# Kernel tuning notes

Hardware: AMD Instinct MI355X
Metric: run time of the kernel (lower is better)

The kernel has to match this reference:

```python
import jax, jax.numpy as jnp
import numpy as np
from jax import lax

SEQ_LEN = 12
E = 64        # embedding_dim
HD = 128      # h_dim
G = 32        # number of scenes (seq_start_end rows)
P = 32        # pedestrians per scene
B = G * P     # total batch
BOT = 1024    # bottleneck_dim
MLP = 1024    # mlp_dim
BN_S = 1.0 / np.sqrt(1.0 + 1e-5)  # eval BatchNorm1d with running mean 0 / var 1


def setup_inputs():
    key = jax.random.key(0)
    ks = jax.random.split(key, 32)
    r = lambda k, s, sc=0.1: (jax.random.normal(k, s, jnp.float32) * sc)
    starts = np.arange(G, dtype=np.int32) * P
    sse = jnp.asarray(np.stack([starts, starts + P], 1))
    return {
        'last_pos': r(ks[0], (B, 2), 1.0),
        'last_pos_rel': r(ks[1], (B, 2), 1.0),
        'h0': r(ks[2], (1, B, HD), 1.0),
        'c0': r(ks[3], (1, B, HD), 1.0),
        'vx': r(ks[4], (8, B), 1.0),
        'vy': r(ks[5], (8, B), 1.0),
        'agent_type': jax.random.uniform(ks[6], (8, B, 1), jnp.float32),
        'seq_start_end': sse,
        # decoder params
        'W_sp': r(ks[7], (2, E)), 'b_sp': r(ks[8], (E,)),
        'W_ih': r(ks[9], (E, 4 * HD)), 'W_hh': r(ks[10], (HD, 4 * HD)),
        'b_ih': r(ks[11], (4 * HD,)), 'b_hh': r(ks[12], (4 * HD,)),
        'W_h2p': r(ks[13], (HD, 2)), 'b_h2p': r(ks[14], (2,)),
        # AttenPoolNet params
        'Wp_sp': r(ks[15], (2, E)), 'bp_sp': r(ks[16], (E,)),
        'Wp_vel': r(ks[17], (2, E)), 'bp_vel': r(ks[18], (E,)),
        'Wp_at': r(ks[19], (6, E)), 'bp_at': r(ks[20], (E,)),
        'Wa1': r(ks[21], (E, MLP)), 'ba1': r(ks[22], (MLP,)),
        'Wa2': r(ks[23], (MLP, 1)), 'ba2': r(ks[24], (1,)),
        'Wm1': r(ks[25], (E + HD, 512)), 'bm1': r(ks[26], (512,)),
        'Wm2': r(ks[27], (512, BOT)), 'bm2': r(ks[28], (BOT,)),
        # decoder post-pool mlp: [h+bottleneck, mlp_dim, h]
        'Wd1': r(ks[29], (HD + BOT, MLP)), 'bd1': r(ks[30], (MLP,)),
        'Wd2': r(ks[31], (MLP, HD)), 'bd2': jnp.zeros((HD,), jnp.float32),
    }


def _bnrelu(x):
    # make_mlp: Linear -> BatchNorm1d (eval, mean 0 / var 1) -> ReLU
    return jax.nn.relu(x * BN_S)


def reference(last_pos, last_pos_rel, h0, c0, vx, vy, agent_type, seq_start_end,
              W_sp, b_sp, W_ih, W_hh, b_ih, b_hh, W_h2p, b_h2p,
              Wp_sp, bp_sp, Wp_vel, bp_vel, Wp_at, bp_at,
              Wa1, ba1, Wa2, ba2, Wm1, bm1, Wm2, bm2,
              Wd1, bd1, Wd2, bd2):
    g = seq_start_end.shape[0]
    p = last_pos.shape[0] // g

    at0 = agent_type[0].reshape(g, p, 1)               # agent_type[0,:,:] per group
    at_rep = jnp.repeat(at0, 6, axis=-1)               # .repeat(num_ped, 6) width expansion
    at_emb = at_rep @ Wp_at + bp_at                    # (g,p,E), index j (tiled over i)
    vel = jnp.stack([vx[-1], vy[-1]], -1).reshape(g, p, 2)
    _vel_emb = vel @ Wp_vel + bp_vel                   # computed in source, unused downstream

    def pool(h2d, pos):
        Hh = h2d.reshape(g, p, HD)
        pg = pos.reshape(g, p, 2)
        # rel[s,i,j] = pos[s,j] - pos[s,i]
        rel = pg[:, None, :, :] - pg[:, :, None, :]
        rel_emb = rel @ Wp_sp + bp_sp                  # (g,p,p,E)
        a = _bnrelu(rel_emb @ Wa1 + ba1)               # (g,p,p,MLP)
        s = _bnrelu(a @ Wa2 + ba2)                     # (g,p,p,1)
        w = jax.nn.softmax(s, axis=-1)                 # torch softmax(dim=1) over size-1 axis -> ones
        base = jnp.concatenate([Hh, at_emb], -1)       # (g,p,192), index j
        wt = base[:, None, :, :] * (0.05 * w)          # (g,p,p,192)
        m = _bnrelu(wt @ Wm1 + bm1)
        m = _bnrelu(m @ Wm2 + bm2)                     # (g,p,p,BOT)
        return m.max(axis=2).reshape(g * p, BOT)       # max over j per tile index i

    def lstm(x, h, c):
        gates = x @ W_ih + h @ W_hh + b_ih + b_hh
        i, f, gg, o = jnp.split(gates, 4, axis=-1)
        c = jax.nn.sigmoid(f) * c + jax.nn.sigmoid(i) * jnp.tanh(gg)
        h = jax.nn.sigmoid(o) * jnp.tanh(c)
        return h, c

    def step(carry, _):
        lp, di, h, c = carry
        h, c = lstm(di, h, c)
        rel = h @ W_h2p + b_h2p
        cur = rel + lp
        ph = pool(h, cur)
        dh = _bnrelu(jnp.concatenate([h, ph], -1) @ Wd1 + bd1)
        dh = _bnrelu(dh @ Wd2 + bd2)
        di = rel @ W_sp + b_sp
        return (cur, di, dh, c), rel

    init = (last_pos, last_pos_rel @ W_sp + b_sp, h0[0], c0[0])
    (lp, di, h, c), rels = lax.scan(step, init, None, length=SEQ_LEN)
    return rels, h[None]  # (seq_len,B,2), (1,B,HD)
```

## Files before the change

kernel.cpp:

```cpp
#include <hip/hip_runtime.h>
#include <math.h>

#define BN_SF 0.9999950000374997f

typedef __attribute__((ext_vector_type(8))) short short8v;
typedef __attribute__((ext_vector_type(4))) float float4v;

__device__ __forceinline__ float sigm(float x) { return 1.0f / (1.0f + expf(-x)); }

__device__ __forceinline__ short f2bf(float x) {
    unsigned u = __builtin_bit_cast(unsigned, x);
    unsigned r = (u + 0x7fffu + ((u >> 16) & 1u)) >> 16;
    return (short)r;
}
__device__ __forceinline__ float bf2f(short h) {
    unsigned u = ((unsigned)(unsigned short)h) << 16;
    return __builtin_bit_cast(float, u);
}

struct SetupP {
    const float *Wm2, *Wd1, *Wd2, *Wm1, *Wih, *Whh, *Wpat, *bpat, *bm1, *c0;
    const float *Wsp, *bsp, *bih, *bhh;
    short *Wm2s, *Wd1f, *Wd2f, *Wm1f, *WghHi, *WghLo;
    float *uv, *cbuf, *fc;
};

__global__ __launch_bounds__(256) void k_setup(SetupP p) {
    __shared__ float tile[32][65];
    __shared__ float rw2[64], su[4][64], sv[4][64];
    int b = blockIdx.x, t = threadIdx.x;

    if (b < 960) {
        const float* src; short* dst; short* dst2 = nullptr;
        int K, N, tm; float scale = 1.f;
        if (b < 256)      { src = p.Wm2; dst = p.Wm2s; K = 512;  N = 1024; tm = b; }
        else if (b < 832) { src = p.Wd1; dst = p.Wd1f; K = 1152; N = 1024; tm = b - 256; }
        else if (b < 896) { src = p.Wd2; dst = p.Wd2f; K = 1024; N = 128;  tm = b - 832; }
        else if (b < 928) { src = p.Wm1; dst = p.Wm1f; K = 128;  N = 512;  tm = b - 896; scale = 0.05f; }
        else              { src = p.Whh; dst = p.WghHi; dst2 = p.WghLo; K = 128; N = 512; tm = b - 928; }
        int tiles_n = N >> 6;
        int kt = tm / tiles_n, nt = tm - kt * tiles_n;
        for (int i = t; i < 2048; i += 256) {
            int r = i >> 6, c = i & 63;
            tile[r][c] = scale * src[(size_t)(kt * 32 + r) * N + nt * 64 + c];
        }
        __syncthreads();
        int lane = t & 63, ntgl = t >> 6;
        int ntg = nt * 4 + ntgl;
        size_t off = (size_t)ntg * ((K >> 5) * 512) + (size_t)kt * 512 + lane * 8;
        int kl = (lane >> 4) << 3, nl = ntgl * 16 + (lane & 15);
        short8v vh, vl;
#pragma unroll
        for (int j = 0; j < 8; ++j) {
            float v = tile[kl + j][nl];
            short hi = f2bf(v);
            vh[j] = hi; vl[j] = f2bf(v - bf2f(hi));
        }
        *(short8v*)(dst + off) = vh;
        if (dst2) *(short8v*)(dst2 + off) = vl;
    } else {
        int i0 = (b - 960) * 256 + t;
        ((float4*)p.cbuf)[i0] = ((const float4*)p.c0)[i0];
        ((float4*)p.cbuf)[i0 + 16384] = ((const float4*)p.c0)[i0 + 16384];
    }

    if (b < 8) {
        int lane = t & 63, seg = t >> 6;
        if (t < 64) { float s = 0.f; for (int k = 0; k < 6; ++k) s += p.Wpat[k * 64 + t]; rw2[t] = s; }
        __syncthreads();
        int c = b * 64 + lane;
        float u = 0.f, v = 0.f;
        for (int e = seg * 16; e < seg * 16 + 16; ++e) {
            float wg = p.Wm1[(size_t)(128 + e) * 512 + c];
            u += rw2[e] * wg; v += p.bpat[e] * wg;
        }
        su[seg][lane] = u; sv[seg][lane] = v;
        __syncthreads();
        if (seg == 0) {
            u = su[0][lane] + su[1][lane] + su[2][lane] + su[3][lane];
            v = sv[0][lane] + sv[1][lane] + sv[2][lane] + sv[3][lane];
            p.uv[c] = 0.05f * u; p.uv[512 + c] = 0.05f * v + p.bm1[c];
        }
    }
    if (b == 8) {
        for (int c = t; c < 512; c += 256) {
            float f0 = 0.f, f1 = 0.f, cc = 0.f;
            for (int e = 0; e < 64; ++e) {
                float wv = p.Wih[(size_t)e * 512 + c];
                f0 += p.Wsp[e] * wv; f1 += p.Wsp[64 + e] * wv; cc += p.bsp[e] * wv;
            }
            p.fc[c] = f0; p.fc[512 + c] = f1; p.fc[1024 + c] = cc + p.bih[c] + p.bhh[c];
        }
    }
}

__global__ __launch_bounds__(512, 4) void k_step(
    const short* __restrict__ WghHi, const short* __restrict__ WghLo,
    const short* __restrict__ Wm1f, const short* __restrict__ Wd2f,
    const short* __restrict__ Wd1f,
    const float* __restrict__ Whp, const float* __restrict__ bhp,
    const float* __restrict__ bd1, const float* __restrict__ bd2,
    const float* __restrict__ at0, const float* __restrict__ uv,
    const float* __restrict__ fc,
    const float* __restrict__ h0, const float* __restrict__ relsrc,
    const float* __restrict__ phwp, const short* __restrict__ hf_in, int first,
    float* __restrict__ cbuf, short* __restrict__ hf_out,
    short* __restrict__ m1s, float* __restrict__ outrel) {
    __shared__ float sgu[16 * 512];
    __shared__ float sh[16][128];
    __shared__ float phws[1024];
    __shared__ short xfh[4 * 512];
    __shared__ short xfl[4 * 512];
    __shared__ short xm[4 * 512];
    __shared__ float srelp[16][2];
    __shared__ float sat[16];
    short* dh1L = (short*)sgu;
    float* sg = sgu;

    int t = threadIdx.x, b = blockIdx.x;
    int l = t & 63, w = t >> 6;
    int s = b >> 1, mt = b & 1, r0 = b * 16;
    int rbase = (l >> 4) << 2;

    if (t < 16) sat[t] = at0[r0 + t];
    if (t < 32) { int row = t >> 1, d = t & 1; srelp[row][d] = relsrc[(r0 + row) * 2 + d]; }

    if (first) {
        for (int i = t; i < 16 * 128; i += 512) sh[i >> 7][i & 127] = h0[r0 * 128 + i];
        __syncthreads();
    } else {
        for (int i = t; i < 1024; i += 512) {
            float v = bd1[i];
#pragma unroll
            for (int ct = 0; ct < 8; ++ct) v += phwp[(size_t)s * 8192 + ct * 1024 + i];
            phws[i] = v;
        }
        __syncthreads();
        short8v Ah[4];
#pragma unroll
        for (int kc = 0; kc < 4; ++kc)
            Ah[kc] = *(const short8v*)(hf_in + (size_t)b * 2048 + kc * 512 + l * 8);
#pragma unroll 1
        for (int q2 = 0; q2 < 4; ++q2) {
            short8v B[2][4];
#pragma unroll
            for (int qq = 0; qq < 2; ++qq)
#pragma unroll
                for (int kc = 0; kc < 4; ++kc)
                    B[qq][kc] = *(const short8v*)(Wd1f + (size_t)(w * 8 + q2 * 2 + qq) * 18432 + kc * 512 + l * 8);
            float4v acc2[2];
#pragma unroll
            for (int qq = 0; qq < 2; ++qq) {
                int col = (w * 8 + q2 * 2 + qq) * 16 + (l & 15);
                float pv = phws[col];
                acc2[qq] = (float4v){pv, pv, pv, pv};
            }
#pragma unroll
            for (int kc = 0; kc < 4; ++kc)
#pragma unroll
                for (int qq = 0; qq < 2; ++qq)
                    acc2[qq] = __builtin_amdgcn_mfma_f32_16x16x32_bf16(Ah[kc], B[qq][kc], acc2[qq], 0, 0, 0);
#pragma unroll
            for (int qq = 0; qq < 2; ++qq) {
                int col = (w * 8 + q2 * 2 + qq) * 16 + (l & 15);
                int kcD = col >> 5, jD = col & 7, lD = ((col & 31) >> 3) << 4;
#pragma unroll
                for (int r = 0; r < 4; ++r) {
                    float v = fmaxf(BN_SF * acc2[qq][r], 0.f);
                    dh1L[kcD * 512 + (rbase + r + lD) * 8 + jD] = f2bf(v);
                }
            }
        }
        __syncthreads();
        float4v hacc = {0.f, 0.f, 0.f, 0.f};
        const short* ap = dh1L + l * 8;
        const short* bp = Wd2f + (size_t)w * 16384 + l * 8;
#pragma unroll 1
        for (int kt = 0; kt < 4; ++kt) {
            short8v B[8], A[8];
#pragma unroll
            for (int kk = 0; kk < 8; ++kk) B[kk] = *(const short8v*)(bp + (kt * 8 + kk) * 512);
#pragma unroll
            for (int kk = 0; kk < 8; ++kk) A[kk] = *(const short8v*)(ap + (kt * 8 + kk) * 512);
#pragma unroll
            for (int kk = 0; kk < 8; ++kk)
                hacc = __builtin_amdgcn_mfma_f32_16x16x32_bf16(A[kk], B[kk], hacc, 0, 0, 0);
        }
        int col = w * 16 + (l & 15);
        float bb2 = bd2[col];
        __syncthreads();
#pragma unroll
        for (int r = 0; r < 4; ++r)
            sh[rbase + r][col] = fmaxf(BN_SF * (hacc[r] + bb2), 0.f);
        __syncthreads();
    }

    for (int i = t; i < 4 * 512; i += 512) {
        int pos = i & 511, kc = i >> 9;
        int ll = pos >> 3, j = pos & 7;
        int row = ll & 15, kh = kc * 32 + ((ll >> 4) << 3) + j;
        float v = sh[row][kh];
        short hi = f2bf(v);
        xfh[i] = hi;
        xfl[i] = f2bf(v - bf2f(hi));
    }
    __syncthreads();

    {
        float4v ga[4];
#pragma unroll
        for (int q = 0; q < 4; ++q) {
            int col = (w * 4 + q) * 16 + (l & 15);
            float f0 = fc[col], f1 = fc[512 + col], cc = fc[1024 + col];
#pragma unroll
            for (int r = 0; r < 4; ++r)
                ga[q][r] = srelp[rbase + r][0] * f0 + srelp[rbase + r][1] * f1 + cc;
        }
#pragma unroll 1
        for (int kt = 0; kt < 2; ++kt) {
            short8v BH[2][4], BL[2][4], AH[2], AL[2];
#pragma unroll
            for (int kk = 0; kk < 2; ++kk) {
                int kcx = kt * 2 + kk;
#pragma unroll
                for (int q = 0; q < 4; ++q) {
                    int nf = w * 4 + q;
                    BH[kk][q] = *(const short8v*)(WghHi + (size_t)nf * 2048 + kcx * 512 + l * 8);
                    BL[kk][q] = *(const short8v*)(WghLo + (size_t)nf * 2048 + kcx * 512 + l * 8);
                }
                AH[kk] = *(const short8v*)(&xfh[kcx * 512 + l * 8]);
                AL[kk] = *(const short8v*)(&xfl[kcx * 512 + l * 8]);
            }
#pragma unroll
            for (int kk = 0; kk < 2; ++kk)
#pragma unroll
                for (int q = 0; q < 4; ++q) {
                    ga[q] = __builtin_amdgcn_mfma_f32_16x16x32_bf16(AH[kk], BH[kk][q], ga[q], 0, 0, 0);
                    ga[q] = __builtin_amdgcn_mfma_f32_16x16x32_bf16(AH[kk], BL[kk][q], ga[q], 0, 0, 0);
                    ga[q] = __builtin_amdgcn_mfma_f32_16x16x32_bf16(AL[kk], BH[kk][q], ga[q], 0, 0, 0);
                }
        }
#pragma unroll
        for (int q = 0; q < 4; ++q) {
            int col = (w * 4 + q) * 16 + (l & 15);
#pragma unroll
            for (int r = 0; r < 4; ++r)
                sg[(rbase + r) * 512 + col] = ga[q][r];
        }
    }
    __syncthreads();

    for (int i = t; i < 16 * 128; i += 512) {
        int row = i >> 7, j = i & 127;
        float gi = sg[row * 512 + j], gf = sg[row * 512 + j + 128];
        float gg = sg[row * 512 + j + 256], go = sg[row * 512 + j + 384];
        float cn = sigm(gf) * cbuf[(r0 + row) * 128 + j] + sigm(gi) * tanhf(gg);
        float hn = sigm(go) * tanhf(cn);
        cbuf[(r0 + row) * 128 + j] = cn;
        sh[row][j] = hn;
    }
    __syncthreads();

    if (t < 256) {
        int row = t >> 4, d = (t >> 3) & 1, seg = t & 7;
        float v = 0.f;
#pragma unroll
        for (int kk = 0; kk < 16; ++kk) {
            int k = seg * 16 + kk;
            v += sh[row][k] * Whp[k * 2 + d];
        }
        v += __shfl_xor(v, 1, 64); v += __shfl_xor(v, 2, 64); v += __shfl_xor(v, 4, 64);
        if (seg == 0) outrel[(r0 + row) * 2 + d] = v + bhp[d];
    }
    for (int i = t; i < 4 * 512; i += 512) {
        int pos = i & 511, kc = i >> 9;
        int ll = pos >> 3, j = pos & 7;
        int row = ll & 15, k = kc * 32 + ((ll >> 4) << 3) + j;
        short hv = f2bf(sh[row][k]);
        xm[i] = hv;
        hf_out[(size_t)b * 2048 + i] = hv;
    }
    __syncthreads();

    {
        float4v ma[4] = {{0,0,0,0},{0,0,0,0},{0,0,0,0},{0,0,0,0}};
        short8v A[4], B[4][4];
#pragma unroll
        for (int kc = 0; kc < 4; ++kc) {
#pragma unroll
            for (int q = 0; q < 4; ++q)
                B[kc][q] = *(const short8v*)(Wm1f + (size_t)(w * 4 + q) * 2048 + kc * 512 + l * 8);
            A[kc] = *(const short8v*)(&xm[kc * 512 + l * 8]);
        }
#pragma unroll
        for (int kc = 0; kc < 4; ++kc)
#pragma unroll
            for (int q = 0; q < 4; ++q)
                ma[q] = __builtin_amdgcn_mfma_f32_16x16x32_bf16(A[kc], B[kc][q], ma[q], 0, 0, 0);
#pragma unroll
        for (int q = 0; q < 4; ++q) {
            int col = (w * 4 + q) * 16 + (l & 15);
            float uc = uv[col], vc = uv[512 + col];
#pragma unroll
            for (int r = 0; r < 4; ++r) {
                int rowC = rbase + r;
                float m1v = fmaxf(BN_SF * (ma[q][r] + sat[rowC] * uc + vc), 0.f);
                int kcD = col >> 5;
                int laneD = rowC + (((col & 31) >> 3) << 4);
                m1s[(size_t)s * 16384 + kcD * 1024 + mt * 512 + laneD * 8 + (col & 7)] = f2bf(m1v);
            }
        }
    }
}

__global__ __launch_bounds__(512, 4) void k_m2(const short* __restrict__ m1s,
                                               const short* __restrict__ Wm2s,
                                               const short* __restrict__ Wd1f,
                                               const float* __restrict__ bm2,
                                               float* __restrict__ phwp) {
    __shared__ short sphb[128];
    int t = threadIdx.x, l = t & 63, w = t >> 6;
    int s = blockIdx.x >> 3, ct = blockIdx.x & 7;

    {
        int nf = ct * 8 + w;
        const short* ap = m1s + (size_t)s * 16384 + l * 8;
        const short* bp = Wm2s + (size_t)nf * 8192 + l * 8;
        float4v acc0 = {0,0,0,0}, acc1 = {0,0,0,0};
#pragma unroll 1
        for (int kt = 0; kt < 4; ++kt) {
            short8v A0[4], A1[4], B[4];
#pragma unroll
            for (int kk = 0; kk < 4; ++kk) {
                int kc = kt * 4 + kk;
                B[kk] = *(const short8v*)(bp + kc * 512);
                A0[kk] = *(const short8v*)(ap + kc * 1024);
                A1[kk] = *(const short8v*)(ap + kc * 1024 + 512);
            }
#pragma unroll
            for (int kk = 0; kk < 4; ++kk) {
                acc0 = __builtin_amdgcn_mfma_f32_16x16x32_bf16(A0[kk], B[kk], acc0, 0, 0, 0);
                acc1 = __builtin_amdgcn_mfma_f32_16x16x32_bf16(A1[kk], B[kk], acc1, 0, 0, 0);
            }
        }
        float m = acc0[0];
#pragma unroll
        for (int ri = 1; ri < 4; ++ri) m = fmaxf(m, acc0[ri]);
#pragma unroll
        for (int ri = 0; ri < 4; ++ri) m = fmaxf(m, acc1[ri]);
        m = fmaxf(m, __shfl_xor(m, 16, 64));
        m = fmaxf(m, __shfl_xor(m, 32, 64));
        if (l < 16) {
            int col = nf * 16 + l;
            sphb[w * 16 + l] = f2bf(fmaxf(BN_SF * (m + bm2[col]), 0.f));
        }
    }
    __syncthreads();

    {
        short8v Ap[4];
#pragma unroll
        for (int kk = 0; kk < 4; ++kk)
            Ap[kk] = *(const short8v*)(sphb + kk * 32 + ((l >> 4) << 3));
#pragma unroll 1
        for (int q2 = 0; q2 < 4; ++q2) {
            short8v B[2][4];
#pragma unroll
            for (int qq = 0; qq < 2; ++qq)
#pragma unroll
                for (int kk = 0; kk < 4; ++kk)
                    B[qq][kk] = *(const short8v*)(Wd1f + (size_t)(w * 8 + q2 * 2 + qq) * 18432
                                                  + (size_t)(4 + ct * 4 + kk) * 512 + l * 8);
            float4v acc2[2] = {{0,0,0,0},{0,0,0,0}};
#pragma unroll
            for (int kk = 0; kk < 4; ++kk)
#pragma unroll
                for (int qq = 0; qq < 2; ++qq)
                    acc2[qq] = __builtin_amdgcn_mfma_f32_16x16x32_bf16(Ap[kk], B[qq][kk], acc2[qq], 0, 0, 0);
            if (l < 16) {
#pragma unroll
                for (int qq = 0; qq < 2; ++qq) {
                    int nf_p = w * 8 + q2 * 2 + qq;
                    phwp[(size_t)s * 8192 + ct * 1024 + nf_p * 16 + l] = acc2[qq][0];
                }
            }
        }
    }
}

__global__ __launch_bounds__(512, 4) void k_hfin(const short* __restrict__ Wd2f,
                                                 const short* __restrict__ Wd1f,
                                                 const float* __restrict__ bd1,
                                                 const float* __restrict__ bd2,
                                                 const float* __restrict__ phwp,
                                                 const short* __restrict__ hf,
                                                 float* __restrict__ outh) {
    __shared__ float phws[1024];
    __shared__ short dh1L[16384];
    int t = threadIdx.x, b = blockIdx.x;
    int l = t & 63, w = t >> 6;
    int s = b >> 1, rbase = (l >> 4) << 2;

    for (int i = t; i < 1024; i += 512) {
        float v = bd1[i];
#pragma unroll
        for (int ct = 0; ct < 8; ++ct) v += phwp[(size_t)s * 8192 + ct * 1024 + i];
        phws[i] = v;
    }
    __syncthreads();
    short8v Ah[4];
#pragma unroll
    for (int kc = 0; kc < 4; ++kc)
        Ah[kc] = *(const short8v*)(hf + (size_t)b * 2048 + kc * 512 + l * 8);
#pragma unroll 1
    for (int q2 = 0; q2 < 4; ++q2) {
        short8v B[2][4];
#pragma unroll
        for (int qq = 0; qq < 2; ++qq)
#pragma unroll
            for (int kc = 0; kc < 4; ++kc)
                B[qq][kc] = *(const short8v*)(Wd1f + (size_t)(w * 8 + q2 * 2 + qq) * 18432 + kc * 512 + l * 8);
        float4v acc2[2];
#pragma unroll
        for (int qq = 0; qq < 2; ++qq) {
            int col = (w * 8 + q2 * 2 + qq) * 16 + (l & 15);
            float pv = phws[col];
            acc2[qq] = (float4v){pv, pv, pv, pv};
        }
#pragma unroll
        for (int kc = 0; kc < 4; ++kc)
#pragma unroll
            for (int qq = 0; qq < 2; ++qq)
                acc2[qq] = __builtin_amdgcn_mfma_f32_16x16x32_bf16(Ah[kc], B[qq][kc], acc2[qq], 0, 0, 0);
#pragma unroll
        for (int qq = 0; qq < 2; ++qq) {
            int col = (w * 8 + q2 * 2 + qq) * 16 + (l & 15);
            int kcD = col >> 5, jD = col & 7, lD = ((col & 31) >> 3) << 4;
#pragma unroll
            for (int r = 0; r < 4; ++r) {
                float v = fmaxf(BN_SF * acc2[qq][r], 0.f);
                dh1L[kcD * 512 + (rbase + r + lD) * 8 + jD] = f2bf(v);
            }
        }
    }
    __syncthreads();
    float4v hacc = {0.f, 0.f, 0.f, 0.f};
    const short* ap = dh1L + l * 8;
    const short* bp = Wd2f + (size_t)w * 16384 + l * 8;
#pragma unroll 1
    for (int kt = 0; kt < 4; ++kt) {
        short8v B[8], A[8];
#pragma unroll
        for (int kk = 0; kk < 8; ++kk) B[kk] = *(const short8v*)(bp + (kt * 8 + kk) * 512);
#pragma unroll
        for (int kk = 0; kk < 8; ++kk) A[kk] = *(const short8v*)(ap + (kt * 8 + kk) * 512);
#pragma unroll
        for (int kk = 0; kk < 8; ++kk)
            hacc = __builtin_amdgcn_mfma_f32_16x16x32_bf16(A[kk], B[kk], hacc, 0, 0, 0);
    }
    int col = w * 16 + (l & 15);
    float bb2 = bd2[col];
#pragma unroll
    for (int r = 0; r < 4; ++r)
        outh[(b * 16 + rbase + r) * 128 + col] = fmaxf(BN_SF * (hacc[r] + bb2), 0.f);
}

extern "C" void kernel_launch(void* const* d_in, const int* in_sizes, int n_in,
                              void* d_out, int out_size, void* d_ws, size_t ws_size,
                              hipStream_t stream) {
    const float* lpr   = (const float*)d_in[1];
    const float* h0    = (const float*)d_in[2];
    const float* c0    = (const float*)d_in[3];
    const float* at0   = (const float*)d_in[6];
    const float* W_sp  = (const float*)d_in[8];
    const float* b_sp  = (const float*)d_in[9];
    const float* W_ih  = (const float*)d_in[10];
    const float* W_hh  = (const float*)d_in[11];
    const float* b_ih  = (const float*)d_in[12];
    const float* b_hh  = (const float*)d_in[13];
    const float* W_h2p = (const float*)d_in[14];
    const float* b_h2p = (const float*)d_in[15];
    const float* Wp_at = (const float*)d_in[20];
    const float* bp_at = (const float*)d_in[21];
    const float* Wm1   = (const float*)d_in[26];
    const float* bm1   = (const float*)d_in[27];
    const float* Wm2   = (const float*)d_in[28];
    const float* bm2   = (const float*)d_in[29];
    const float* Wd1   = (const float*)d_in[30];
    const float* bd1   = (const float*)d_in[31];
    const float* Wd2   = (const float*)d_in[32];
    const float* bd2   = (const float*)d_in[33];
    float* out = (float*)d_out;

    float* ws    = (float*)d_ws;
    float* uv    = ws;
    float* fc    = uv + 1024;
    float* cbuf  = fc + 1536;
    float* phwp  = cbuf + 131072;
    short* hf    = (short*)(phwp + 262144);
    short* m1s   = hf + 131072;
    short* Wm2s  = m1s + 524288;
    short* Wd1f  = Wm2s + 524288;
    short* Wd2f  = Wd1f + 1179648;
    short* Wm1f  = Wd2f + 131072;
    short* WghHi = Wm1f + 65536;
    short* WghLo = WghHi + 65536;

    SetupP sp;
    sp.Wm2 = Wm2; sp.Wd1 = Wd1; sp.Wd2 = Wd2; sp.Wm1 = Wm1;
    sp.Wih = W_ih; sp.Whh = W_hh; sp.Wpat = Wp_at; sp.bpat = bp_at; sp.bm1 = bm1;
    sp.c0 = c0; sp.Wsp = W_sp; sp.bsp = b_sp; sp.bih = b_ih; sp.bhh = b_hh;
    sp.Wm2s = Wm2s; sp.Wd1f = Wd1f; sp.Wd2f = Wd2f;
    sp.Wm1f = Wm1f; sp.WghHi = WghHi; sp.WghLo = WghLo;
    sp.uv = uv; sp.cbuf = cbuf; sp.fc = fc;

    k_setup<<<1024, 256, 0, stream>>>(sp);

    for (int t = 0; t < 12; ++t) {
        const float* relsrc = (t == 0) ? lpr : (out + (size_t)(t - 1) * 2048);
        k_step<<<64, 512, 0, stream>>>(WghHi, WghLo, Wm1f, Wd2f, Wd1f,
                                       W_h2p, b_h2p, bd1, bd2, at0, uv, fc,
                                       h0, relsrc, phwp, hf, (t == 0) ? 1 : 0,
                                       cbuf, hf, m1s, out + (size_t)t * 2048);
        k_m2<<<256, 512, 0, stream>>>(m1s, Wm2s, Wd1f, bm2, phwp);
    }
    k_hfin<<<64, 512, 0, stream>>>(Wd2f, Wd1f, bd1, bd2, phwp, hf, out + 24576);
}
```

Before: 328.3 us.

## Fuse per-step kernels into one persistent kernel with flag-based inter-block sync

```diff
diff --git a/kernel.cpp b/kernel.cpp
--- a/kernel.cpp
+++ b/kernel.cpp
@@ -16,6 +16,33 @@
 __device__ __forceinline__ float bf2f(short h) {
     unsigned u = ((unsigned)(unsigned short)h) << 16;
     return __builtin_bit_cast(float, u);
+}
+
+__device__ __forceinline__ void st_ag64(void* p, unsigned long long v) {
+    __hip_atomic_store((unsigned long long*)p, v, __ATOMIC_RELAXED, __HIP_MEMORY_SCOPE_AGENT);
+}
+__device__ __forceinline__ unsigned long long ld_ag64(const void* p) {
+    return __hip_atomic_load((const unsigned long long*)p, __ATOMIC_RELAXED, __HIP_MEMORY_SCOPE_AGENT);
+}
+__device__ __forceinline__ void st_ag32f(float* p, float v) {
+    __hip_atomic_store((unsigned*)p, __builtin_bit_cast(unsigned, v), __ATOMIC_RELAXED, __HIP_MEMORY_SCOPE_AGENT);
+}
+__device__ __forceinline__ short8v ld_ag_frag(const short* p) {
+    unsigned long long a = ld_ag64(p), c = ld_ag64(p + 4);
+    short8v v;
+    ((unsigned long long*)&v)[0] = a;
+    ((unsigned long long*)&v)[1] = c;
+    return v;
+}
+__device__ __forceinline__ void waitge(int* f, int target) {
+    long it = 0;
+    while (__hip_atomic_load(f, __ATOMIC_RELAXED, __HIP_MEMORY_SCOPE_AGENT) < target) {
+        __builtin_amdgcn_s_sleep(1);
+        if (++it > (1L << 26)) break;
+    }
+}
+__device__ __forceinline__ void bump_release(int* f) {
+    __hip_atomic_fetch_add(f, 1, __ATOMIC_RELEASE, __HIP_MEMORY_SCOPE_AGENT);
 }
 
 struct SetupP {
@@ -23,6 +50,7 @@
     const float *Wsp, *bsp, *bih, *bhh;
     short *Wm2s, *Wd1f, *Wd2f, *Wm1f, *WghHi, *WghLo;
     float *uv, *cbuf, *fc;
+    int *flags;
 };
 
 __global__ __launch_bounds__(256) void k_setup(SetupP p) {
@@ -92,54 +120,342 @@
             p.fc[c] = f0; p.fc[512 + c] = f1; p.fc[1024 + c] = cc + p.bih[c] + p.bhh[c];
         }
     }
-}
-
-__global__ __launch_bounds__(512, 4) void k_step(
-    const short* __restrict__ WghHi, const short* __restrict__ WghLo,
-    const short* __restrict__ Wm1f, const short* __restrict__ Wd2f,
-    const short* __restrict__ Wd1f,
-    const float* __restrict__ Whp, const float* __restrict__ bhp,
-    const float* __restrict__ bd1, const float* __restrict__ bd2,
-    const float* __restrict__ at0, const float* __restrict__ uv,
-    const float* __restrict__ fc,
-    const float* __restrict__ h0, const float* __restrict__ relsrc,
-    const float* __restrict__ phwp, const short* __restrict__ hf_in, int first,
-    float* __restrict__ cbuf, short* __restrict__ hf_out,
-    short* __restrict__ m1s, float* __restrict__ outrel) {
+    if (b == 9) {
+        if (t < 64) p.flags[t] = 0;
+    }
+}
+
+struct PersistP {
+    const short *WghHi, *WghLo, *Wm1f, *Wd2f, *Wd1f, *Wm2s;
+    const float *Whp, *bhp, *bd1, *bd2, *at0, *uv, *fc, *h0, *lpr, *bm2;
+    float *cbuf;
+    short *hf;
+    short *m1s;
+    float *phwp;
+    int *m1rdy, *phwrdy;
+    float *out;
+};
+
+__global__ __launch_bounds__(512) void k_persist(PersistP p) {
     __shared__ float sgu[16 * 512];
     __shared__ float sh[16][128];
     __shared__ float phws[1024];
-    __shared__ short xfh[4 * 512];
-    __shared__ short xfl[4 * 512];
-    __shared__ short xm[4 * 512];
+    __shared__ short xfh[2048];
+    __shared__ short xfl[2048];
+    __shared__ short xm[2048];
     __shared__ float srelp[16][2];
     __shared__ float sat[16];
+    __shared__ short sphb[128];
     short* dh1L = (short*)sgu;
     float* sg = sgu;
+    short* m1stage = (short*)sgu;
 
     int t = threadIdx.x, b = blockIdx.x;
     int l = t & 63, w = t >> 6;
+    int rbase = (l >> 4) << 2;
+    int s2 = b >> 3, ct = b & 7;
+    bool isStep = (b < 64);
     int s = b >> 1, mt = b & 1, r0 = b * 16;
-    int rbase = (l >> 4) << 2;
-
-    if (t < 16) sat[t] = at0[r0 + t];
-    if (t < 32) { int row = t >> 1, d = t & 1; srelp[row][d] = relsrc[(r0 + row) * 2 + d]; }
-
-    if (first) {
-        for (int i = t; i < 16 * 128; i += 512) sh[i >> 7][i & 127] = h0[r0 * 128 + i];
-        __syncthreads();
-    } else {
-        for (int i = t; i < 1024; i += 512) {
-            float v = bd1[i];
-#pragma unroll
-            for (int ct = 0; ct < 8; ++ct) v += phwp[(size_t)s * 8192 + ct * 1024 + i];
-            phws[i] = v;
+
+    if (isStep && t < 16) sat[t] = p.at0[r0 + t];
+
+    for (int st = 0; st < 12; ++st) {
+        if (isStep) {
+            if (st == 0) {
+                for (int i = t; i < 2048; i += 512) sh[i >> 7][i & 127] = p.h0[r0 * 128 + i];
+                if (t < 32) { int row = t >> 1, d = t & 1; srelp[row][d] = p.lpr[(r0 + row) * 2 + d]; }
+                __syncthreads();
+            } else {
+                if (t == 0) waitge(p.phwrdy + s, 8 * st);
+                __syncthreads();
+                {
+                    float a0 = p.bd1[t * 2], a1 = p.bd1[t * 2 + 1];
+#pragma unroll
+                    for (int cc = 0; cc < 8; ++cc) {
+                        unsigned long long v = ld_ag64(&p.phwp[(size_t)s * 8192 + cc * 1024 + t * 2]);
+                        float2 f = __builtin_bit_cast(float2, v);
+                        a0 += f.x; a1 += f.y;
+                    }
+                    phws[t * 2] = a0; phws[t * 2 + 1] = a1;
+                }
+                if (t < 32) {
+                    int row = t >> 1, d = t & 1;
+                    srelp[row][d] = p.out[(size_t)(st - 1) * 2048 + (r0 + row) * 2 + d];
+                }
+                __syncthreads();
+                short8v Ah[4];
+#pragma unroll
+                for (int kc = 0; kc < 4; ++kc)
+                    Ah[kc] = *(const short8v*)(p.hf + (size_t)b * 2048 + kc * 512 + l * 8);
+#pragma unroll 1
+                for (int q2 = 0; q2 < 4; ++q2) {
+                    short8v B[2][4];
+#pragma unroll
+                    for (int qq = 0; qq < 2; ++qq)
+#pragma unroll
+                        for (int kc = 0; kc < 4; ++kc)
+                            B[qq][kc] = *(const short8v*)(p.Wd1f + (size_t)(w * 8 + q2 * 2 + qq) * 18432 + kc * 512 + l * 8);
+                    float4v acc2[2];
+#pragma unroll
+                    for (int qq = 0; qq < 2; ++qq) {
+                        int col = (w * 8 + q2 * 2 + qq) * 16 + (l & 15);
+                        float pv = phws[col];
+                        acc2[qq] = (float4v){pv, pv, pv, pv};
+                    }
+#pragma unroll
+                    for (int kc = 0; kc < 4; ++kc)
+#pragma unroll
+                        for (int qq = 0; qq < 2; ++qq)
+                            acc2[qq] = __builtin_amdgcn_mfma_f32_16x16x32_bf16(Ah[kc], B[qq][kc], acc2[qq], 0, 0, 0);
+#pragma unroll
+                    for (int qq = 0; qq < 2; ++qq) {
+                        int col = (w * 8 + q2 * 2 + qq) * 16 + (l & 15);
+                        int kcD = col >> 5, jD = col & 7, lD = ((col & 31) >> 3) << 4;
+#pragma unroll
+                        for (int r = 0; r < 4; ++r) {
+                            float v = fmaxf(BN_SF * acc2[qq][r], 0.f);
+                            dh1L[kcD * 512 + (rbase + r + lD) * 8 + jD] = f2bf(v);
+                        }
+                    }
+                }
+                __syncthreads();
+                float4v hacc = {0.f, 0.f, 0.f, 0.f};
+                const short* ap = dh1L + l * 8;
+                const short* bp = p.Wd2f + (size_t)w * 16384 + l * 8;
+#pragma unroll 1
+                for (int kt = 0; kt < 4; ++kt) {
+                    short8v B[8], A[8];
+#pragma unroll
+                    for (int kk = 0; kk < 8; ++kk) B[kk] = *(const short8v*)(bp + (kt * 8 + kk) * 512);
+#pragma unroll
+                    for (int kk = 0; kk < 8; ++kk) A[kk] = *(const short8v*)(ap + (kt * 8 + kk) * 512);
+#pragma unroll
+                    for (int kk = 0; kk < 8; ++kk)
+                        hacc = __builtin_amdgcn_mfma_f32_16x16x32_bf16(A[kk], B[kk], hacc, 0, 0, 0);
+                }
+                int col = w * 16 + (l & 15);
+                float bb2 = p.bd2[col];
+                __syncthreads();
+#pragma unroll
+                for (int r = 0; r < 4; ++r)
+                    sh[rbase + r][col] = fmaxf(BN_SF * (hacc[r] + bb2), 0.f);
+                __syncthreads();
+            }
+
+            for (int i = t; i < 2048; i += 512) {
+                int pos = i & 511, kc = i >> 9;
+                int ll = pos >> 3, j = pos & 7;
+                int row = ll & 15, kh = kc * 32 + ((ll >> 4) << 3) + j;
+                float v = sh[row][kh];
+                short hi = f2bf(v);
+                xfh[i] = hi;
+                xfl[i] = f2bf(v - bf2f(hi));
+            }
+            __syncthreads();
+
+            {
+                float4v ga[4];
+#pragma unroll
+                for (int qg = 0; qg < 4; ++qg) {
+                    int col = (w * 4 + qg) * 16 + (l & 15);
+                    float f0 = p.fc[col], f1 = p.fc[512 + col], cc = p.fc[1024 + col];
+#pragma unroll
+                    for (int r = 0; r < 4; ++r)
+                        ga[qg][r] = srelp[rbase + r][0] * f0 + srelp[rbase + r][1] * f1 + cc;
+                }
+#pragma unroll 1
+                for (int kt = 0; kt < 2; ++kt) {
+                    short8v BH[2][4], BL[2][4], AH[2], AL[2];
+#pragma unroll
+                    for (int kk = 0; kk < 2; ++kk) {
+                        int kcx = kt * 2 + kk;
+#pragma unroll
+                        for (int qg = 0; qg < 4; ++qg) {
+                            int nf = w * 4 + qg;
+                            BH[kk][qg] = *(const short8v*)(p.WghHi + (size_t)nf * 2048 + kcx * 512 + l * 8);
+                            BL[kk][qg] = *(const short8v*)(p.WghLo + (size_t)nf * 2048 + kcx * 512 + l * 8);
+                        }
+                        AH[kk] = *(const short8v*)(&xfh[kcx * 512 + l * 8]);
+                        AL[kk] = *(const short8v*)(&xfl[kcx * 512 + l * 8]);
+                    }
+#pragma unroll
+                    for (int kk = 0; kk < 2; ++kk)
+#pragma unroll
+                        for (int qg = 0; qg < 4; ++qg) {
+                            ga[qg] = __builtin_amdgcn_mfma_f32_16x16x32_bf16(AH[kk], BH[kk][qg], ga[qg], 0, 0, 0);
+                            ga[qg] = __builtin_amdgcn_mfma_f32_16x16x32_bf16(AH[kk], BL[kk][qg], ga[qg], 0, 0, 0);
+                            ga[qg] = __builtin_amdgcn_mfma_f32_16x16x32_bf16(AL[kk], BH[kk][qg], ga[qg], 0, 0, 0);
+                        }
+                }
+#pragma unroll
+                for (int qg = 0; qg < 4; ++qg) {
+                    int col = (w * 4 + qg) * 16 + (l & 15);
+#pragma unroll
+                    for (int r = 0; r < 4; ++r)
+                        sg[(rbase + r) * 512 + col] = ga[qg][r];
+                }
+            }
+            __syncthreads();
+
+            for (int i = t; i < 2048; i += 512) {
+                int row = i >> 7, j = i & 127;
+                float gi = sg[row * 512 + j], gf = sg[row * 512 + j + 128];
+                float gg = sg[row * 512 + j + 256], go = sg[row * 512 + j + 384];
+                float cn = sigm(gf) * p.cbuf[(r0 + row) * 128 + j] + sigm(gi) * tanhf(gg);
+                float hn = sigm(go) * tanhf(cn);
+                p.cbuf[(r0 + row) * 128 + j] = cn;
+                sh[row][j] = hn;
+            }
+            __syncthreads();
+
+            if (t < 256) {
+                int row = t >> 4, d = (t >> 3) & 1, seg = t & 7;
+                float v = 0.f;
+#pragma unroll
+                for (int kk = 0; kk < 16; ++kk) {
+                    int k = seg * 16 + kk;
+                    v += sh[row][k] * p.Whp[k * 2 + d];
+                }
+                v += __shfl_xor(v, 1, 64); v += __shfl_xor(v, 2, 64); v += __shfl_xor(v, 4, 64);
+                if (seg == 0) p.out[(size_t)st * 2048 + (r0 + row) * 2 + d] = v + p.bhp[d];
+            }
+            for (int i = t; i < 2048; i += 512) {
+                int pos = i & 511, kc = i >> 9;
+                int ll = pos >> 3, j = pos & 7;
+                int row = ll & 15, k = kc * 32 + ((ll >> 4) << 3) + j;
+                short hv = f2bf(sh[row][k]);
+                xm[i] = hv;
+                p.hf[(size_t)b * 2048 + i] = hv;
+            }
+            __syncthreads();
+
+            {
+                float4v ma[4] = {{0,0,0,0},{0,0,0,0},{0,0,0,0},{0,0,0,0}};
+                short8v A[4], B[4][4];
+#pragma unroll
+                for (int kc = 0; kc < 4; ++kc) {
+#pragma unroll
+                    for (int qg = 0; qg < 4; ++qg)
+                        B[kc][qg] = *(const short8v*)(p.Wm1f + (size_t)(w * 4 + qg) * 2048 + kc * 512 + l * 8);
+                    A[kc] = *(const short8v*)(&xm[kc * 512 + l * 8]);
+                }
+#pragma unroll
+                for (int kc = 0; kc < 4; ++kc)
+#pragma unroll
+                    for (int qg = 0; qg < 4; ++qg)
+                        ma[qg] = __builtin_amdgcn_mfma_f32_16x16x32_bf16(A[kc], B[kc][qg], ma[qg], 0, 0, 0);
+#pragma unroll
+                for (int qg = 0; qg < 4; ++qg) {
+                    int col = (w * 4 + qg) * 16 + (l & 15);
+                    float uc = p.uv[col], vc = p.uv[512 + col];
+#pragma unroll
+                    for (int r = 0; r < 4; ++r) {
+                        int rowC = rbase + r;
+                        float m1v = fmaxf(BN_SF * (ma[qg][r] + sat[rowC] * uc + vc), 0.f);
+                        int kcD = col >> 5;
+                        int laneD = rowC + (((col & 31) >> 3) << 4);
+                        m1stage[kcD * 512 + laneD * 8 + (col & 7)] = f2bf(m1v);
+                    }
+                }
+            }
+            __syncthreads();
+            for (int i = t; i < 2048; i += 512) {
+                int kcD = i >> 7, off = (i & 127) * 4;
+                st_ag64(p.m1s + (size_t)s * 16384 + (size_t)kcD * 1024 + mt * 512 + off,
+                        ((const unsigned long long*)m1stage)[i]);
+            }
+            __syncthreads();
+            if (t == 0) bump_release(p.m1rdy + s);
+        }
+
+        if (t == 0) waitge(p.m1rdy + s2, 2 * (st + 1));
+        __syncthreads();
+        {
+            int nf = ct * 8 + w;
+            const short* ap = p.m1s + (size_t)s2 * 16384 + l * 8;
+            const short* bp = p.Wm2s + (size_t)nf * 8192 + l * 8;
+            float4v acc0 = {0,0,0,0}, acc1 = {0,0,0,0};
+#pragma unroll 1
+            for (int kt = 0; kt < 4; ++kt) {
+                short8v A0[4], A1[4], B[4];
+#pragma unroll
+                for (int kk = 0; kk < 4; ++kk) {
+                    int kc = kt * 4 + kk;
+                    B[kk] = *(const short8v*)(bp + kc * 512);
+                    A0[kk] = ld_ag_frag(ap + kc * 1024);
+                    A1[kk] = ld_ag_frag(ap + kc * 1024 + 512);
+                }
+#pragma unroll
+                for (int kk = 0; kk < 4; ++kk) {
+                    acc0 = __builtin_amdgcn_mfma_f32_16x16x32_bf16(A0[kk], B[kk], acc0, 0, 0, 0);
+                    acc1 = __builtin_amdgcn_mfma_f32_16x16x32_bf16(A1[kk], B[kk], acc1, 0, 0, 0);
+                }
+            }
+            float m = acc0[0];
+#pragma unroll
+            for (int ri = 1; ri < 4; ++ri) m = fmaxf(m, acc0[ri]);
+#pragma unroll
+            for (int ri = 0; ri < 4; ++ri) m = fmaxf(m, acc1[ri]);
+            m = fmaxf(m, __shfl_xor(m, 16, 64));
+            m = fmaxf(m, __shfl_xor(m, 32, 64));
+            if (l < 16) {
+                int colx = nf * 16 + l;
+                sphb[w * 16 + l] = f2bf(fmaxf(BN_SF * (m + p.bm2[colx]), 0.f));
+            }
+        }
+        __syncthreads();
+        {
+            short8v Ap[4];
+#pragma unroll
+            for (int kk = 0; kk < 4; ++kk)
+                Ap[kk] = *(const short8v*)(sphb + kk * 32 + ((l >> 4) << 3));
+#pragma unroll 1
+            for (int q2 = 0; q2 < 4; ++q2) {
+                short8v B[2][4];
+#pragma unroll
+                for (int qq = 0; qq < 2; ++qq)
+#pragma unroll
+                    for (int kk = 0; kk < 4; ++kk)
+                        B[qq][kk] = *(const short8v*)(p.Wd1f + (size_t)(w * 8 + q2 * 2 + qq) * 18432
+                                                      + (size_t)(4 + ct * 4 + kk) * 512 + l * 8);
+                float4v acc2[2] = {{0,0,0,0},{0,0,0,0}};
+#pragma unroll
+                for (int kk = 0; kk < 4; ++kk)
+#pragma unroll
+                    for (int qq = 0; qq < 2; ++qq)
+                        acc2[qq] = __builtin_amdgcn_mfma_f32_16x16x32_bf16(Ap[kk], B[qq][kk], acc2[qq], 0, 0, 0);
+                if (l < 16) {
+#pragma unroll
+                    for (int qq = 0; qq < 2; ++qq) {
+                        int nf_p = w * 8 + q2 * 2 + qq;
+                        st_ag32f(&p.phwp[(size_t)s2 * 8192 + ct * 1024 + nf_p * 16 + l], acc2[qq][0]);
+                    }
+                }
+            }
+        }
+        __syncthreads();
+        if (t == 0) bump_release(p.phwrdy + s2);
+        __syncthreads();
+    }
+
+    if (isStep) {
+        if (t == 0) waitge(p.phwrdy + s, 96);
+        __syncthreads();
+        {
+            float a0 = p.bd1[t * 2], a1 = p.bd1[t * 2 + 1];
+#pragma unroll
+            for (int cc = 0; cc < 8; ++cc) {
+                unsigned long long v = ld_ag64(&p.phwp[(size_t)s * 8192 + cc * 1024 + t * 2]);
+                float2 f = __builtin_bit_cast(float2, v);
+                a0 += f.x; a1 += f.y;
+            }
+            phws[t * 2] = a0; phws[t * 2 + 1] = a1;
         }
         __syncthreads();
         short8v Ah[4];
 #pragma unroll
         for (int kc = 0; kc < 4; ++kc)
-            Ah[kc] = *(const short8v*)(hf_in + (size_t)b * 2048 + kc * 512 + l * 8);
+            Ah[kc] = *(const short8v*)(p.hf + (size_t)b * 2048 + kc * 512 + l * 8);
 #pragma unroll 1
         for (int q2 = 0; q2 < 4; ++q2) {
             short8v B[2][4];
@@ -147,7 +463,7 @@
             for (int qq = 0; qq < 2; ++qq)
 #pragma unroll
                 for (int kc = 0; kc < 4; ++kc)
-                    B[qq][kc] = *(const short8v*)(Wd1f + (size_t)(w * 8 + q2 * 2 + qq) * 18432 + kc * 512 + l * 8);
+                    B[qq][kc] = *(const short8v*)(p.Wd1f + (size_t)(w * 8 + q2 * 2 + qq) * 18432 + kc * 512 + l * 8);
             float4v acc2[2];
 #pragma unroll
             for (int qq = 0; qq < 2; ++qq) {
@@ -174,7 +490,7 @@
         __syncthreads();
         float4v hacc = {0.f, 0.f, 0.f, 0.f};
         const short* ap = dh1L + l * 8;
-        const short* bp = Wd2f + (size_t)w * 16384 + l * 8;
+        const short* bp = p.Wd2f + (size_t)w * 16384 + l * 8;
 #pragma unroll 1
         for (int kt = 0; kt < 4; ++kt) {
             short8v B[8], A[8];
@@ -187,282 +503,12 @@
                 hacc = __builtin_amdgcn_mfma_f32_16x16x32_bf16(A[kk], B[kk], hacc, 0, 0, 0);
         }
         int col = w * 16 + (l & 15);
-        float bb2 = bd2[col];
-        __syncthreads();
+        float bb2 = p.bd2[col];
 #pragma unroll
         for (int r = 0; r < 4; ++r)
-            sh[rbase + r][col] = fmaxf(BN_SF * (hacc[r] + bb2), 0.f);
-        __syncthreads();
-    }
-
-    for (int i = t; i < 4 * 512; i += 512) {
-        int pos = i & 511, kc = i >> 9;
-        int ll = pos >> 3, j = pos & 7;
-        int row = ll & 15, kh = kc * 32 + ((ll >> 4) << 3) + j;
-        float v = sh[row][kh];
-        short hi = f2bf(v);
-        xfh[i] = hi;
-        xfl[i] = f2bf(v - bf2f(hi));
-    }
-    __syncthreads();
-
-    {
-        float4v ga[4];
-#pragma unroll
-        for (int q = 0; q < 4; ++q) {
-            int col = (w * 4 + q) * 16 + (l & 15);
-            float f0 = fc[col], f1 = fc[512 + col], cc = fc[1024 + col];
-#pragma unroll
-            for (int r = 0; r < 4; ++r)
-                ga[q][r] = srelp[rbase + r][0] * f0 + srelp[rbase + r][1] * f1 + cc;
-        }
-#pragma unroll 1
-        for (int kt = 0; kt < 2; ++kt) {
-            short8v BH[2][4], BL[2][4], AH[2], AL[2];
-#pragma unroll
-            for (int kk = 0; kk < 2; ++kk) {
-                int kcx = kt * 2 + kk;
-#pragma unroll
-                for (int q = 0; q < 4; ++q) {
-                    int nf = w * 4 + q;
-                    BH[kk][q] = *(const short8v*)(WghHi + (size_t)nf * 2048 + kcx * 512 + l * 8);
-                    BL[kk][q] = *(const short8v*)(WghLo + (size_t)nf * 2048 + kcx * 512 + l * 8);
-                }
-                AH[kk] = *(const short8v*)(&xfh[kcx * 512 + l * 8]);
-                AL[kk] = *(const short8v*)(&xfl[kcx * 512 + l * 8]);
-            }
-#pragma unroll
-            for (int kk = 0; kk < 2; ++kk)
-#pragma unroll
-                for (int q = 0; q < 4; ++q) {
-                    ga[q] = __builtin_amdgcn_mfma_f32_16x16x32_bf16(AH[kk], BH[kk][q], ga[q], 0, 0, 0);
-                    ga[q] = __builtin_amdgcn_mfma_f32_16x16x32_bf16(AH[kk], BL[kk][q], ga[q], 0, 0, 0);
-                    ga[q] = __builtin_amdgcn_mfma_f32_16x16x32_bf16(AL[kk], BH[kk][q], ga[q], 0, 0, 0);
-                }
-        }
-#pragma unroll
-        for (int q = 0; q < 4; ++q) {
-            int col = (w * 4 + q) * 16 + (l & 15);
-#pragma unroll
-            for (int r = 0; r < 4; ++r)
-                sg[(rbase + r) * 512 + col] = ga[q][r];
-        }
-    }
-    __syncthreads();
-
-    for (int i = t; i < 16 * 128; i += 512) {
-        int row = i >> 7, j = i & 127;
-        float gi = sg[row * 512 + j], gf = sg[row * 512 + j + 128];
-        float gg = sg[row * 512 + j + 256], go = sg[row * 512 + j + 384];
-        float cn = sigm(gf) * cbuf[(r0 + row) * 128 + j] + sigm(gi) * tanhf(gg);
-        float hn = sigm(go) * tanhf(cn);
-        cbuf[(r0 + row) * 128 + j] = cn;
-        sh[row][j] = hn;
-    }
-    __syncthreads();
-
-    if (t < 256) {
-        int row = t >> 4, d = (t >> 3) & 1, seg = t & 7;
-        float v = 0.f;
-#pragma unroll
-        for (int kk = 0; kk < 16; ++kk) {
-            int k = seg * 16 + kk;
-            v += sh[row][k] * Whp[k * 2 + d];
-        }
-        v += __shfl_xor(v, 1, 64); v += __shfl_xor(v, 2, 64); v += __shfl_xor(v, 4, 64);
-        if (seg == 0) outrel[(r0 + row) * 2 + d] = v + bhp[d];
-    }
-    for (int i = t; i < 4 * 512; i += 512) {
-        int pos = i & 511, kc = i >> 9;
-        int ll = pos >> 3, j = pos & 7;
-        int row = ll & 15, k = kc * 32 + ((ll >> 4) << 3) + j;
-        short hv = f2bf(sh[row][k]);
-        xm[i] = hv;
-        hf_out[(size_t)b * 2048 + i] = hv;
-    }
-    __syncthreads();
-
-    {
-        float4v ma[4] = {{0,0,0,0},{0,0,0,0},{0,0,0,0},{0,0,0,0}};
-        short8v A[4], B[4][4];
-#pragma unroll
-        for (int kc = 0; kc < 4; ++kc) {
-#pragma unroll
-            for (int q = 0; q < 4; ++q)
-                B[kc][q] = *(const short8v*)(Wm1f + (size_t)(w * 4 + q) * 2048 + kc * 512 + l * 8);
-            A[kc] = *(const short8v*)(&xm[kc * 512 + l * 8]);
-        }
-#pragma unroll
-        for (int kc = 0; kc < 4; ++kc)
-#pragma unroll
-            for (int q = 0; q < 4; ++q)
-                ma[q] = __builtin_amdgcn_mfma_f32_16x16x32_bf16(A[kc], B[kc][q], ma[q], 0, 0, 0);
-#pragma unroll
-        for (int q = 0; q < 4; ++q) {
-            int col = (w * 4 + q) * 16 + (l & 15);
-            float uc = uv[col], vc = uv[512 + col];
-#pragma unroll
-            for (int r = 0; r < 4; ++r) {
-                int rowC = rbase + r;
-                float m1v = fmaxf(BN_SF * (ma[q][r] + sat[rowC] * uc + vc), 0.f);
-                int kcD = col >> 5;
-                int laneD = rowC + (((col & 31) >> 3) << 4);
-                m1s[(size_t)s * 16384 + kcD * 1024 + mt * 512 + laneD * 8 + (col & 7)] = f2bf(m1v);
-            }
-        }
-    }
-}
-
-__global__ __launch_bounds__(512, 4) void k_m2(const short* __restrict__ m1s,
-                                               const short* __restrict__ Wm2s,
-                                               const short* __restrict__ Wd1f,
-                                               const float* __restrict__ bm2,
-                                               float* __restrict__ phwp) {
-    __shared__ short sphb[128];
-    int t = threadIdx.x, l = t & 63, w = t >> 6;
-    int s = blockIdx.x >> 3, ct = blockIdx.x & 7;
-
-    {
-        int nf = ct * 8 + w;
-        const short* ap = m1s + (size_t)s * 16384 + l * 8;
-        const short* bp = Wm2s + (size_t)nf * 8192 + l * 8;
-        float4v acc0 = {0,0,0,0}, acc1 = {0,0,0,0};
-#pragma unroll 1
-        for (int kt = 0; kt < 4; ++kt) {
-            short8v A0[4], A1[4], B[4];
-#pragma unroll
-            for (int kk = 0; kk < 4; ++kk) {
-                int kc = kt * 4 + kk;
-                B[kk] = *(const short8v*)(bp + kc * 512);
-                A0[kk] = *(const short8v*)(ap + kc * 1024);
-                A1[kk] = *(const short8v*)(ap + kc * 1024 + 512);
-            }
-#pragma unroll
-            for (int kk = 0; kk < 4; ++kk) {
-                acc0 = __builtin_amdgcn_mfma_f32_16x16x32_bf16(A0[kk], B[kk], acc0, 0, 0, 0);
-                acc1 = __builtin_amdgcn_mfma_f32_16x16x32_bf16(A1[kk], B[kk], acc1, 0, 0, 0);
-            }
-        }
-        float m = acc0[0];
-#pragma unroll
-        for (int ri = 1; ri < 4; ++ri) m = fmaxf(m, acc0[ri]);
-#pragma unroll
-        for (int ri = 0; ri < 4; ++ri) m = fmaxf(m, acc1[ri]);
-        m = fmaxf(m, __shfl_xor(m, 16, 64));
-        m = fmaxf(m, __shfl_xor(m, 32, 64));
-        if (l < 16) {
-            int col = nf * 16 + l;
-            sphb[w * 16 + l] = f2bf(fmaxf(BN_SF * (m + bm2[col]), 0.f));
-        }
-    }
-    __syncthreads();
-
-    {
-        short8v Ap[4];
-#pragma unroll
-        for (int kk = 0; kk < 4; ++kk)
-            Ap[kk] = *(const short8v*)(sphb + kk * 32 + ((l >> 4) << 3));
-#pragma unroll 1
-        for (int q2 = 0; q2 < 4; ++q2) {
-            short8v B[2][4];
-#pragma unroll
-            for (int qq = 0; qq < 2; ++qq)
-#pragma unroll
-                for (int kk = 0; kk < 4; ++kk)
-                    B[qq][kk] = *(const short8v*)(Wd1f + (size_t)(w * 8 + q2 * 2 + qq) * 18432
-                                                  + (size_t)(4 + ct * 4 + kk) * 512 + l * 8);
-            float4v acc2[2] = {{0,0,0,0},{0,0,0,0}};
-#pragma unroll
-            for (int kk = 0; kk < 4; ++kk)
-#pragma unroll
-                for (int qq = 0; qq < 2; ++qq)
-                    acc2[qq] = __builtin_amdgcn_mfma_f32_16x16x32_bf16(Ap[kk], B[qq][kk], acc2[qq], 0, 0, 0);
-            if (l < 16) {
-#pragma unroll
-                for (int qq = 0; qq < 2; ++qq) {
-                    int nf_p = w * 8 + q2 * 2 + qq;
-                    phwp[(size_t)s * 8192 + ct * 1024 + nf_p * 16 + l] = acc2[qq][0];
-                }
-            }
-        }
-    }
-}
-
-__global__ __launch_bounds__(512, 4) void k_hfin(const short* __restrict__ Wd2f,
-                                                 const short* __restrict__ Wd1f,
-                                                 const float* __restrict__ bd1,
-                                                 const float* __restrict__ bd2,
-                                                 const float* __restrict__ phwp,
-                                                 const short* __restrict__ hf,
-                                                 float* __restrict__ outh) {
-    __shared__ float phws[1024];
-    __shared__ short dh1L[16384];
-    int t = threadIdx.x, b = blockIdx.x;
-    int l = t & 63, w = t >> 6;
-    int s = b >> 1, rbase = (l >> 4) << 2;
-
-    for (int i = t; i < 1024; i += 512) {
-        float v = bd1[i];
-#pragma unroll
-        for (int ct = 0; ct < 8; ++ct) v += phwp[(size_t)s * 8192 + ct * 1024 + i];
-        phws[i] = v;
-    }
-    __syncthreads();
-    short8v Ah[4];
-#pragma unroll
-    for (int kc = 0; kc < 4; ++kc)
-        Ah[kc] = *(const short8v*)(hf + (size_t)b * 2048 + kc * 512 + l * 8);
-#pragma unroll 1
-    for (int q2 = 0; q2 < 4; ++q2) {
-        short8v B[2][4];
-#pragma unroll
-        for (int qq = 0; qq < 2; ++qq)
-#pragma unroll
-            for (int kc = 0; kc < 4; ++kc)
-                B[qq][kc] = *(const short8v*)(Wd1f + (size_t)(w * 8 + q2 * 2 + qq) * 18432 + kc * 512 + l * 8);
-        float4v acc2[2];
-#pragma unroll
-        for (int qq = 0; qq < 2; ++qq) {
-            int col = (w * 8 + q2 * 2 + qq) * 16 + (l & 15);
-            float pv = phws[col];
-            acc2[qq] = (float4v){pv, pv, pv, pv};
-        }
-#pragma unroll
-        for (int kc = 0; kc < 4; ++kc)
-#pragma unroll
-            for (int qq = 0; qq < 2; ++qq)
-                acc2[qq] = __builtin_amdgcn_mfma_f32_16x16x32_bf16(Ah[kc], B[qq][kc], acc2[qq], 0, 0, 0);
-#pragma unroll
-        for (int qq = 0; qq < 2; ++qq) {
-            int col = (w * 8 + q2 * 2 + qq) * 16 + (l & 15);
-            int kcD = col >> 5, jD = col & 7, lD = ((col & 31) >> 3) << 4;
-#pragma unroll
-            for (int r = 0; r < 4; ++r) {
-                float v = fmaxf(BN_SF * acc2[qq][r], 0.f);
-                dh1L[kcD * 512 + (rbase + r + lD) * 8 + jD] = f2bf(v);
-            }
-        }
-    }
-    __syncthreads();
-    float4v hacc = {0.f, 0.f, 0.f, 0.f};
-    const short* ap = dh1L + l * 8;
-    const short* bp = Wd2f + (size_t)w * 16384 + l * 8;
-#pragma unroll 1
-    for (int kt = 0; kt < 4; ++kt) {
-        short8v B[8], A[8];
-#pragma unroll
-        for (int kk = 0; kk < 8; ++kk) B[kk] = *(const short8v*)(bp + (kt * 8 + kk) * 512);
-#pragma unroll
-        for (int kk = 0; kk < 8; ++kk) A[kk] = *(const short8v*)(ap + (kt * 8 + kk) * 512);
-#pragma unroll
-        for (int kk = 0; kk < 8; ++kk)
-            hacc = __builtin_amdgcn_mfma_f32_16x16x32_bf16(A[kk], B[kk], hacc, 0, 0, 0);
-    }
-    int col = w * 16 + (l & 15);
-    float bb2 = bd2[col];
-#pragma unroll
-    for (int r = 0; r < 4; ++r)
-        outh[(b * 16 + rbase + r) * 128 + col] = fmaxf(BN_SF * (hacc[r] + bb2), 0.f);
+            p.out[24576 + (size_t)(b * 16 + rbase + r) * 128 + col] =
+                fmaxf(BN_SF * (hacc[r] + bb2), 0.f);
+    }
 }
 
 extern "C" void kernel_launch(void* const* d_in, const int* in_sizes, int n_in,
@@ -497,7 +543,8 @@
     float* fc    = uv + 1024;
     float* cbuf  = fc + 1536;
     float* phwp  = cbuf + 131072;
-    short* hf    = (short*)(phwp + 262144);
+    int*   flags = (int*)(phwp + 262144);
+    short* hf    = (short*)(flags + 64);
     short* m1s   = hf + 131072;
     short* Wm2s  = m1s + 524288;
     short* Wd1f  = Wm2s + 524288;
@@ -512,17 +559,18 @@
     sp.c0 = c0; sp.Wsp = W_sp; sp.bsp = b_sp; sp.bih = b_ih; sp.bhh = b_hh;
     sp.Wm2s = Wm2s; sp.Wd1f = Wd1f; sp.Wd2f = Wd2f;
     sp.Wm1f = Wm1f; sp.WghHi = WghHi; sp.WghLo = WghLo;
-    sp.uv = uv; sp.cbuf = cbuf; sp.fc = fc;
+    sp.uv = uv; sp.cbuf = cbuf; sp.fc = fc; sp.flags = flags;
 
     k_setup<<<1024, 256, 0, stream>>>(sp);
 
-    for (int t = 0; t < 12; ++t) {
-        const float* relsrc = (t == 0) ? lpr : (out + (size_t)(t - 1) * 2048);
-        k_step<<<64, 512, 0, stream>>>(WghHi, WghLo, Wm1f, Wd2f, Wd1f,
-                                       W_h2p, b_h2p, bd1, bd2, at0, uv, fc,
-                                       h0, relsrc, phwp, hf, (t == 0) ? 1 : 0,
-                                       cbuf, hf, m1s, out + (size_t)t * 2048);
-        k_m2<<<256, 512, 0, stream>>>(m1s, Wm2s, Wd1f, bm2, phwp);
-    }
-    k_hfin<<<64, 512, 0, stream>>>(Wd2f, Wd1f, bd1, bd2, phwp, hf, out + 24576);
-}
+    PersistP pp;
+    pp.WghHi = WghHi; pp.WghLo = WghLo; pp.Wm1f = Wm1f; pp.Wd2f = Wd2f;
+    pp.Wd1f = Wd1f; pp.Wm2s = Wm2s;
+    pp.Whp = W_h2p; pp.bhp = b_h2p; pp.bd1 = bd1; pp.bd2 = bd2;
+    pp.at0 = at0; pp.uv = uv; pp.fc = fc; pp.h0 = h0; pp.lpr = lpr; pp.bm2 = bm2;
+    pp.cbuf = cbuf; pp.hf = hf; pp.m1s = m1s; pp.phwp = phwp;
+    pp.m1rdy = flags; pp.phwrdy = flags + 32;
+    pp.out = out;
+
+    k_persist<<<256, 512, 0, stream>>>(pp);
+}
```

Result: slower. 490.8 us (+49.5%).
